# Optimization experiments

Hardware: AMD Instinct MI355X
Metric: run time of the kernel (lower is better)

The kernel has to match this reference:

```python
import jax, jax.numpy as jnp
import numpy as np

WIDTH = 768
HEAD = 64

def setup_inputs() -> dict:
    key = jax.random.key(0)
    ks = jax.random.split(key, 8)
    x = jax.random.normal(ks[0], (8, 2048, WIDTH), dtype=jnp.float32)
    mask = jax.random.randint(ks[1], (2048, 2048), 0, 2, dtype=jnp.int32)
    s = 1.0 / np.sqrt(WIDTH)
    Wq = jax.random.normal(ks[2], (WIDTH, HEAD), dtype=jnp.float32) * s
    Wk = jax.random.normal(ks[3], (WIDTH, HEAD), dtype=jnp.float32) * s
    Wv = jax.random.normal(ks[4], (WIDTH, HEAD), dtype=jnp.float32) * s
    bq = jax.random.normal(ks[5], (HEAD,), dtype=jnp.float32) * 0.01
    bk = jax.random.normal(ks[6], (HEAD,), dtype=jnp.float32) * 0.01
    bv = jax.random.normal(ks[7], (HEAD,), dtype=jnp.float32) * 0.01
    return {"x": x, "Wq": Wq, "bq": bq, "Wk": Wk, "bk": bk, "Wv": Wv, "bv": bv, "mask": mask}

def reference(x, Wq, bq, Wk, bk, Wv, bv, mask) -> jnp.ndarray:
    # x: [B, N, width]; projections -> [B, N, head]
    Q = jnp.einsum('bnw,wh->bnh', x, Wq) + bq
    K = jnp.einsum('bnw,wh->bnh', x, Wk) + bk
    V = jnp.einsum('bnw,wh->bnh', x, Wv) + bv
    scale = 1.0 / jnp.sqrt(jnp.asarray(Q.shape[-1], dtype=Q.dtype))
    scores = jnp.einsum('bqh,bkh->bqk', Q, K) * scale  # [B, N, N]
    scores = jnp.where(mask == 0, -jnp.inf, scores)
    attn = jax.nn.softmax(scores, axis=-1)
    return jnp.einsum('bqk,bkh->bqh', attn, V)
```

## Files before the change

kernel.cpp:

```cpp
#include <hip/hip_runtime.h>

typedef short  s8v   __attribute__((ext_vector_type(8)));
typedef float  f32x4 __attribute__((ext_vector_type(4)));

#define SEQ 2048
#define WID 768

__device__ __forceinline__ unsigned fbits(float f) {
    union { float f; unsigned u; } v; v.f = f; return v.u;
}
__device__ __forceinline__ float bitsf(unsigned u) {
    union { unsigned u; float f; } v; v.u = u; return v.f;
}
__device__ __forceinline__ unsigned short f2b(float f) {
    unsigned u = fbits(f);
    return (unsigned short)((u + 0x7FFFu + ((u >> 16) & 1u)) >> 16);
}
__device__ __forceinline__ unsigned packRNE(float a, float b) {
    unsigned ta = fbits(a) + 0x7FFFu + ((fbits(a) >> 16) & 1u);
    unsigned tb = fbits(b) + 0x7FFFu + ((fbits(b) >> 16) & 1u);
    return __builtin_amdgcn_perm(tb, ta, 0x07060302u);
}
__device__ __forceinline__ unsigned packTRUNC(float a, float b) {
    return __builtin_amdgcn_perm(fbits(b), fbits(a), 0x07060302u);
}
__device__ __forceinline__ f32x4 zero4() { f32x4 z = {0.f, 0.f, 0.f, 0.f}; return z; }

__device__ __forceinline__ void async16(const unsigned short* g, unsigned short* l) {
    __builtin_amdgcn_global_load_lds(
        (const __attribute__((address_space(1))) unsigned int*)g,
        (__attribute__((address_space(3))) unsigned int*)l, 16, 0, 0);
}

__global__ __launch_bounds__(256) void convert_kernel(
    const int* __restrict__ mask,
    const float* __restrict__ Wq, const float* __restrict__ Wk, const float* __restrict__ Wv,
    unsigned short* __restrict__ WF, unsigned* __restrict__ PM)
{
    const int tid = threadIdx.x;
    const int blk = blockIdx.x;
    if (blk < 512) {
        const int gid  = blk * 4 + (tid >> 6);
        const int lane = tid & 63, quad = lane >> 4, c = lane & 15;
        const int qb = gid >> 5, kb = gid & 31;
        unsigned w = 0;
        #pragma unroll
        for (int mt = 0; mt < 2; ++mt) {
            const int q = qb * 32 + mt * 16 + c;
            #pragma unroll
            for (int i = 0; i < 4; ++i) {
                const int4 mm = *(const int4*)&mask[(size_t)q * SEQ + kb * 64 + quad * 16 + 4 * i];
                if (mm.x) w |= 1u << (mt * 16 + i * 4 + 0);
                if (mm.y) w |= 1u << (mt * 16 + i * 4 + 1);
                if (mm.z) w |= 1u << (mt * 16 + i * 4 + 2);
                if (mm.w) w |= 1u << (mt * 16 + i * 4 + 3);
            }
        }
        PM[(size_t)gid * 64 + lane] = w;
    } else {
        const int s2 = (blk - 512) * 256 + tid;
        const int chunk = s2 >> 6, l = s2 & 63;
        const int ntg = chunk / 24, r = chunk - ntg * 24;
        const int kc = r >> 1, h = r & 1;
        const int mat = ntg >> 2;
        const int col = (ntg & 3) * 16 + (l & 15);
        const int k0 = kc * 64 + h * 32 + (l >> 4) * 8;
        const float* Wm = (mat == 0) ? Wq : (mat == 1) ? Wk : Wv;
        float p[8];
        #pragma unroll
        for (int j = 0; j < 8; ++j) p[j] = Wm[(size_t)(k0 + j) * 64 + col];
        uint4 w;
        w.x = packRNE(p[0], p[1]); w.y = packRNE(p[2], p[3]);
        w.z = packRNE(p[4], p[5]); w.w = packRNE(p[6], p[7]);
        *(uint4*)&WF[(size_t)s2 * 8] = w;
    }
}

__global__ __launch_bounds__(512, 4) void qkv_proj_kernel(
    const float* __restrict__ x, const unsigned short* __restrict__ WF,
    const float* __restrict__ bq, const float* __restrict__ bk, const float* __restrict__ bv,
    unsigned short* __restrict__ QF, unsigned short* __restrict__ KF,
    unsigned short* __restrict__ VF)
{
    __shared__ unsigned short AB[2][16384];
    unsigned short (*St)[200] = (unsigned short(*)[200])AB;

    const int tid = threadIdx.x;
    const int wv = tid >> 6, lane = tid & 63, quad = lane >> 4, c = lane & 15;
    const int rg = wv >> 2, cg = wv & 3;
    const int blk = blockIdx.x;
    const int g0 = blk * 4;

    float bias[3];
    #pragma unroll
    for (int nt = 0; nt < 3; ++nt) {
        int col = cg * 48 + nt * 16 + c;
        const float* B = (col < 64) ? bq : (col < 128) ? bk : bv;
        bias[nt] = B[col & 63];
    }

    const int chunk = tid >> 6;
    const int gl = chunk >> 1, hh = chunk & 1;
    const int arow = (g0 + gl) * 16 + (lane & 15);
    const float* xrow = x + (size_t)arow * WID + hh * 32 + ((lane >> 4) & 3) * 8;

    auto issueB = [&](int kc, int b) {
        #pragma unroll
        for (int r = 0; r < 3; ++r) {
            const int e = wv * 3 + r;
            const int ntg = e >> 1, h = e & 1;
            async16(WF + (((size_t)ntg * 12 + kc) * 2 + h) * 512 + lane * 8,
                    &AB[b][4096 + (ntg * 2 + h) * 512]);
        }
    };
    auto stageA_write = [&](int b, float4 f0, float4 f1) {
        uint4 w;
        w.x = packRNE(f0.x, f0.y); w.y = packRNE(f0.z, f0.w);
        w.z = packRNE(f1.x, f1.y); w.w = packRNE(f1.z, f1.w);
        *(uint4*)&AB[b][(size_t)tid * 8] = w;
    };

    f32x4 acc[2][3];
    #pragma unroll
    for (int mt = 0; mt < 2; ++mt)
        #pragma unroll
        for (int nt = 0; nt < 3; ++nt) acc[mt][nt] = zero4();

    {
        float4 f0 = *(const float4*)&xrow[0];
        float4 f1 = *(const float4*)&xrow[4];
        stageA_write(0, f0, f1);
        issueB(0, 0);
    }

    for (int kc = 0; kc < 12; ++kc) {
        const int b = kc & 1;
        __syncthreads();
        float4 f0, f1;
        if (kc < 11) {
            f0 = *(const float4*)&xrow[(kc + 1) * 64];
            f1 = *(const float4*)&xrow[(kc + 1) * 64 + 4];
            issueB(kc + 1, b ^ 1);
        }

        s8v afr[2][2], bfr[3][2];
        #pragma unroll
        for (int mt = 0; mt < 2; ++mt)
            #pragma unroll
            for (int h = 0; h < 2; ++h)
                afr[mt][h] = *(const s8v*)&AB[b][((rg * 2 + mt) * 2 + h) * 512 + lane * 8];
        #pragma unroll
        for (int nt = 0; nt < 3; ++nt)
            #pragma unroll
            for (int h = 0; h < 2; ++h)
                bfr[nt][h] = *(const s8v*)&AB[b][4096 + ((cg * 3 + nt) * 2 + h) * 512 + lane * 8];
        #pragma unroll
        for (int h = 0; h < 2; ++h)
            #pragma unroll
            for (int mt = 0; mt < 2; ++mt)
                #pragma unroll
                for (int nt = 0; nt < 3; ++nt)
                    acc[mt][nt] = __builtin_amdgcn_mfma_f32_16x16x32_bf16(
                        afr[mt][h], bfr[nt][h], acc[mt][nt], 0, 0, 0);

        if (kc < 11) stageA_write(b ^ 1, f0, f1);
    }

    #pragma unroll
    for (int mt = 0; mt < 2; ++mt)
        #pragma unroll
        for (int nt = 0; nt < 3; ++nt)
            #pragma unroll
            for (int i = 0; i < 4; ++i)
                St[rg * 32 + mt * 16 + quad * 4 + i][cg * 48 + nt * 16 + c]
                    = f2b(acc[mt][nt][i] + bias[nt]);
    __syncthreads();

    {
        const int g = tid >> 7, ks = (tid >> 6) & 1, l = tid & 63;
        uint4 v = *(uint4*)&St[g * 16 + (l & 15)][ks * 32 + (l >> 4) * 8];
        *(uint4*)&QF[(((size_t)(g0 + g)) * 2 + ks) * 512 + (size_t)l * 8] = v;
    }
    {
        const int ksnt = tid >> 6, l = tid & 63;
        const int ks = ksnt >> 2, nt = ksnt & 3;
        uint4 v = *(uint4*)&St[4 * (l & 15) + nt][64 + ks * 32 + (l >> 4) * 8];
        *(uint4*)&KF[(((size_t)blk * 8 + ksnt) * 64 + l) * 8] = v;
    }
    {
        const int ksnt = tid >> 6, l = tid & 63;
        const int ks = ksnt >> 2, nt = ksnt & 3;
        const int d = 128 + nt * 16 + (l & 15);
        const int r0 = (l >> 4) * 16 + ks * 8;
        unsigned short p[8];
        #pragma unroll
        for (int s = 0; s < 8; ++s) p[s] = St[r0 + s][d];
        uint4 w;
        w.x = (unsigned)p[0] | ((unsigned)p[1] << 16);
        w.y = (unsigned)p[2] | ((unsigned)p[3] << 16);
        w.z = (unsigned)p[4] | ((unsigned)p[5] << 16);
        w.w = (unsigned)p[6] | ((unsigned)p[7] << 16);
        *(uint4*)&VF[(((size_t)blk * 8 + ksnt) * 64 + l) * 8] = w;
    }
}

__global__ __launch_bounds__(1024, 4) void attn_kernel(
    const unsigned short* __restrict__ QF, const unsigned short* __restrict__ KF,
    const unsigned short* __restrict__ VF, const unsigned* __restrict__ PM,
    float* __restrict__ out)
{
    __shared__ unsigned short KV[4][2][8192];
    __shared__ float Obuf[64][68];
    __shared__ float Lbuf[64];

    const int tid = threadIdx.x;
    const int wv = tid >> 6, lane = tid & 63, quad = lane >> 4, c = lane & 15;
    const int sl = wv & 3, qg = wv >> 2, mt = qg & 1;
    const int blk = blockIdx.x;
    const int bb = blk & 7, qt = blk >> 3;
    const size_t qrow0 = (size_t)bb * SEQ + qt * 64;

    if (tid < 64) Lbuf[tid] = 0.f;

    unsigned pm[8];
    #pragma unroll
    for (int kt = 0; kt < 8; ++kt)
        pm[kt] = PM[(size_t)(((qt * 2 + (qg >> 1)) * 32 + sl * 8 + kt) * 64 + lane)];

    union Q8 { s8v v; unsigned w[4]; } qf[2];
    {
        const size_t qgrp = (size_t)bb * 128 + qt * 4 + qg;
        #pragma unroll
        for (int ks = 0; ks < 2; ++ks)
            qf[ks].v = *(const s8v*)&QF[(qgrp * 2 + ks) * 512 + (size_t)lane * 8];
    }
    asm volatile("s_waitcnt vmcnt(0)" ::: "memory");
    #pragma unroll
    for (int kt = 0; kt < 8; ++kt) asm volatile("" : "+v"(pm[kt]));
    #pragma unroll
    for (int ks = 0; ks < 2; ++ks)
        #pragma unroll
        for (int j = 0; j < 4; ++j) asm volatile("" : "+v"(qf[ks].w[j]));
    __builtin_amdgcn_sched_barrier(0);

    f32x4 O[4];
    float lro = 0.f;
    #pragma unroll
    for (int nt = 0; nt < 4; ++nt) O[nt] = zero4();

    auto kv_dma = [&](int kt, int b) {
        const size_t kbg = (size_t)bb * 32 + sl * 8 + kt;
        #pragma unroll
        for (int r = 0; r < 4; ++r) {
            const int d = qg * 4 + r;
            const unsigned short* src = (d < 8)
                ? KF + kbg * 4096 + (d & 7) * 512 + lane * 8
                : VF + kbg * 4096 + (d & 7) * 512 + lane * 8;
            async16(src, &KV[sl][b][(d >> 3) * 4096 + (d & 7) * 512]);
        }
    };

    kv_dma(0, 0);
    kv_dma(1, 1);

    #pragma unroll
    for (int kt = 0; kt < 8; ++kt) {
        const int b = kt & 1;
        if (kt < 7) asm volatile("s_waitcnt vmcnt(4)" ::: "memory");
        else        asm volatile("s_waitcnt vmcnt(0)" ::: "memory");
        __builtin_amdgcn_sched_barrier(0);
        __builtin_amdgcn_s_barrier();

        f32x4 S[4];
        #pragma unroll
        for (int nt = 0; nt < 4; ++nt) S[nt] = zero4();
        #pragma unroll
        for (int ks = 0; ks < 2; ++ks) {
            s8v kfr[4];
            #pragma unroll
            for (int nt = 0; nt < 4; ++nt)
                kfr[nt] = *(const s8v*)&KV[sl][b][((ks * 4 + nt) * 64 + lane) * 8];
            #pragma unroll
            for (int nt = 0; nt < 4; ++nt)
                S[nt] = __builtin_amdgcn_mfma_f32_16x16x32_bf16(kfr[nt], qf[ks].v, S[nt], 0, 0, 0);
        }

        const unsigned pmh = pm[kt] >> (mt * 16);
        float p[4][4];
        #pragma unroll
        for (int i = 0; i < 4; ++i)
            #pragma unroll
            for (int nt = 0; nt < 4; ++nt) {
                float e = exp2f(fmaf(S[nt][i], 0.18033688011112042f, -21.640425613334451f));
                p[nt][i] = ((pmh >> (i * 4 + nt)) & 1u) ? e : 0.f;
            }
        union { unsigned w[8]; s8v v[2]; } P;
        #pragma unroll
        for (int j = 0; j < 8; ++j) {
            unsigned uu = packTRUNC(p[2 * (j & 1)][j >> 1], p[2 * (j & 1) + 1][j >> 1]);
            P.w[j] = uu;
            lro += bitsf(uu << 16) + bitsf(uu & 0xFFFF0000u);
        }

        #pragma unroll
        for (int ks = 0; ks < 2; ++ks) {
            s8v vfr[4];
            #pragma unroll
            for (int nt = 0; nt < 4; ++nt)
                vfr[nt] = *(const s8v*)&KV[sl][b][4096 + ((ks * 4 + nt) * 64 + lane) * 8];
            #pragma unroll
            for (int nt = 0; nt < 4; ++nt)
                O[nt] = __builtin_amdgcn_mfma_f32_16x16x32_bf16(P.v[ks], vfr[nt], O[nt], 0, 0, 0);
        }

        if (kt < 6) {
            __builtin_amdgcn_s_barrier();
            kv_dma(kt + 2, b);
        }
    }

    #pragma unroll
    for (int j = 0; j < 5; ++j) {
        int idx = tid + 1024 * j;
        if (idx < 64 * 68) ((float*)Obuf)[idx] = 0.f;
    }
    __syncthreads();

    {
        float l = lro;
        l += __shfl_xor(l, 16);
        l += __shfl_xor(l, 32);
        if (quad == 0) atomicAdd(&Lbuf[qg * 16 + c], l);
    }
    #pragma unroll
    for (int i = 0; i < 4; ++i)
        #pragma unroll
        for (int nt = 0; nt < 4; ++nt)
            atomicAdd(&Obuf[qg * 16 + quad * 4 + i][nt * 16 + c], O[nt][i]);
    __syncthreads();
    {
        const int r = tid >> 4, d4 = (tid & 15) * 4;
        const float invL = 1.0f / Lbuf[r];
        float4 v = *(float4*)&Obuf[r][d4];
        float4 o = make_float4(v.x * invL, v.y * invL, v.z * invL, v.w * invL);
        *(float4*)&out[(qrow0 + r) * 64 + d4] = o;
    }
}

extern "C" void kernel_launch(void* const* d_in, const int* in_sizes, int n_in,
                              void* d_out, int out_size, void* d_ws, size_t ws_size,
                              hipStream_t stream)
{
    const float* x    = (const float*)d_in[0];
    const float* Wq   = (const float*)d_in[1];
    const float* bq   = (const float*)d_in[2];
    const float* Wk   = (const float*)d_in[3];
    const float* bk   = (const float*)d_in[4];
    const float* Wv   = (const float*)d_in[5];
    const float* bv   = (const float*)d_in[6];
    const int*   mask = (const int*)d_in[7];
    float* out = (float*)d_out;

    unsigned short* QF = (unsigned short*)d_ws;
    unsigned short* KF = QF + (size_t)16384 * 64;
    unsigned short* VF = KF + (size_t)16384 * 64;
    unsigned short* WF = VF + (size_t)16384 * 64;
    unsigned*       PM = (unsigned*)(WF + (size_t)192 * WID);

    convert_kernel<<<584, 256, 0, stream>>>(mask, Wq, Wk, Wv, WF, PM);
    qkv_proj_kernel<<<256, 512, 0, stream>>>(x, WF, bq, bk, bv, QF, KF, VF);
    attn_kernel<<<256, 1024, 0, stream>>>(QF, KF, VF, PM, out);
}
```

Baseline: 159.5 us.

## Fuse convert, QKV projection and attention into one cooperative kernel

Merges the three separate launches (mask/weight conversion, QKV projection, attention) into a single kernel that runs each phase in turn. The phases are separated by a software grid-wide barrier built on an atomic counter, and the kernel is launched cooperatively, with a plain launch as fallback. The shared-memory buffers of the phases are aliased onto one static array. The aim is to remove inter-kernel launch gaps and the drain/fill between phases. In exchange it adds a memset and two spin-wait barriers, and half the threads sit idle during the projection phase. It also depends on all 256 blocks being co-resident, which with about 145 KB of LDS per block means one block per CU.

```diff
diff --git a/kernel.cpp b/kernel.cpp
--- a/kernel.cpp
+++ b/kernel.cpp
@@ -32,318 +32,334 @@
         (__attribute__((address_space(3))) unsigned int*)l, 16, 0, 0);
 }
 
-__global__ __launch_bounds__(256) void convert_kernel(
-    const int* __restrict__ mask,
+__device__ __forceinline__ void grid_barrier(unsigned* bar) {
+    __syncthreads();
+    if (threadIdx.x == 0) {
+        __threadfence();
+        unsigned my  = atomicAdd(bar, 1u);
+        unsigned gen = my >> 8;
+        volatile unsigned* vb = bar;
+        while ((*vb >> 8) <= gen) __builtin_amdgcn_s_sleep(2);
+        __threadfence();
+    }
+    __syncthreads();
+}
+
+__global__ __launch_bounds__(1024, 4) void fused_kernel(
+    const float* __restrict__ x, const int* __restrict__ mask,
     const float* __restrict__ Wq, const float* __restrict__ Wk, const float* __restrict__ Wv,
-    unsigned short* __restrict__ WF, unsigned* __restrict__ PM)
-{
-    const int tid = threadIdx.x;
-    const int blk = blockIdx.x;
-    if (blk < 512) {
-        const int gid  = blk * 4 + (tid >> 6);
-        const int lane = tid & 63, quad = lane >> 4, c = lane & 15;
-        const int qb = gid >> 5, kb = gid & 31;
-        unsigned w = 0;
-        #pragma unroll
-        for (int mt = 0; mt < 2; ++mt) {
-            const int q = qb * 32 + mt * 16 + c;
-            #pragma unroll
-            for (int i = 0; i < 4; ++i) {
-                const int4 mm = *(const int4*)&mask[(size_t)q * SEQ + kb * 64 + quad * 16 + 4 * i];
-                if (mm.x) w |= 1u << (mt * 16 + i * 4 + 0);
-                if (mm.y) w |= 1u << (mt * 16 + i * 4 + 1);
-                if (mm.z) w |= 1u << (mt * 16 + i * 4 + 2);
-                if (mm.w) w |= 1u << (mt * 16 + i * 4 + 3);
-            }
-        }
-        PM[(size_t)gid * 64 + lane] = w;
-    } else {
-        const int s2 = (blk - 512) * 256 + tid;
-        const int chunk = s2 >> 6, l = s2 & 63;
-        const int ntg = chunk / 24, r = chunk - ntg * 24;
-        const int kc = r >> 1, h = r & 1;
-        const int mat = ntg >> 2;
-        const int col = (ntg & 3) * 16 + (l & 15);
-        const int k0 = kc * 64 + h * 32 + (l >> 4) * 8;
-        const float* Wm = (mat == 0) ? Wq : (mat == 1) ? Wk : Wv;
-        float p[8];
-        #pragma unroll
-        for (int j = 0; j < 8; ++j) p[j] = Wm[(size_t)(k0 + j) * 64 + col];
-        uint4 w;
-        w.x = packRNE(p[0], p[1]); w.y = packRNE(p[2], p[3]);
-        w.z = packRNE(p[4], p[5]); w.w = packRNE(p[6], p[7]);
-        *(uint4*)&WF[(size_t)s2 * 8] = w;
-    }
-}
-
-__global__ __launch_bounds__(512, 4) void qkv_proj_kernel(
-    const float* __restrict__ x, const unsigned short* __restrict__ WF,
     const float* __restrict__ bq, const float* __restrict__ bk, const float* __restrict__ bv,
     unsigned short* __restrict__ QF, unsigned short* __restrict__ KF,
-    unsigned short* __restrict__ VF)
+    unsigned short* __restrict__ VF, unsigned short* __restrict__ WF,
+    unsigned* __restrict__ PM, float* __restrict__ out, unsigned* __restrict__ bar)
 {
-    __shared__ unsigned short AB[2][16384];
-    unsigned short (*St)[200] = (unsigned short(*)[200])AB;
+    __shared__ __align__(16) unsigned char SMEM[148736];
 
     const int tid = threadIdx.x;
     const int wv = tid >> 6, lane = tid & 63, quad = lane >> 4, c = lane & 15;
-    const int rg = wv >> 2, cg = wv & 3;
     const int blk = blockIdx.x;
-    const int g0 = blk * 4;
-
-    float bias[3];
-    #pragma unroll
-    for (int nt = 0; nt < 3; ++nt) {
-        int col = cg * 48 + nt * 16 + c;
-        const float* B = (col < 64) ? bq : (col < 128) ? bk : bv;
-        bias[nt] = B[col & 63];
+
+    {
+        const int gw = blk * 16 + wv;
+        if (gw < 2048) {
+            const int gid = gw;
+            const int qb = gid >> 5, kb = gid & 31;
+            unsigned w = 0;
+            #pragma unroll
+            for (int mt = 0; mt < 2; ++mt) {
+                const int q = qb * 32 + mt * 16 + c;
+                #pragma unroll
+                for (int i = 0; i < 4; ++i) {
+                    const int4 mm = *(const int4*)&mask[(size_t)q * SEQ + kb * 64 + quad * 16 + 4 * i];
+                    if (mm.x) w |= 1u << (mt * 16 + i * 4 + 0);
+                    if (mm.y) w |= 1u << (mt * 16 + i * 4 + 1);
+                    if (mm.z) w |= 1u << (mt * 16 + i * 4 + 2);
+                    if (mm.w) w |= 1u << (mt * 16 + i * 4 + 3);
+                }
+            }
+            PM[(size_t)gid * 64 + lane] = w;
+        } else if (gw < 2336) {
+            const int chunk = gw - 2048;
+            const int ntg = chunk / 24, r = chunk - ntg * 24;
+            const int kc = r >> 1, h = r & 1;
+            const int mat = ntg >> 2;
+            const int col = (ntg & 3) * 16 + c;
+            const int k0 = kc * 64 + h * 32 + (lane >> 4) * 8;
+            const float* Wm = (mat == 0) ? Wq : (mat == 1) ? Wk : Wv;
+            float p[8];
+            #pragma unroll
+            for (int j = 0; j < 8; ++j) p[j] = Wm[(size_t)(k0 + j) * 64 + col];
+            uint4 w;
+            w.x = packRNE(p[0], p[1]); w.y = packRNE(p[2], p[3]);
+            w.z = packRNE(p[4], p[5]); w.w = packRNE(p[6], p[7]);
+            *(uint4*)&WF[(size_t)(chunk * 64 + lane) * 8] = w;
+        }
     }
 
-    const int chunk = tid >> 6;
-    const int gl = chunk >> 1, hh = chunk & 1;
-    const int arow = (g0 + gl) * 16 + (lane & 15);
-    const float* xrow = x + (size_t)arow * WID + hh * 32 + ((lane >> 4) & 3) * 8;
-
-    auto issueB = [&](int kc, int b) {
-        #pragma unroll
-        for (int r = 0; r < 3; ++r) {
-            const int e = wv * 3 + r;
-            const int ntg = e >> 1, h = e & 1;
-            async16(WF + (((size_t)ntg * 12 + kc) * 2 + h) * 512 + lane * 8,
-                    &AB[b][4096 + (ntg * 2 + h) * 512]);
-        }
-    };
-    auto stageA_write = [&](int b, float4 f0, float4 f1) {
-        uint4 w;
-        w.x = packRNE(f0.x, f0.y); w.y = packRNE(f0.z, f0.w);
-        w.z = packRNE(f1.x, f1.y); w.w = packRNE(f1.z, f1.w);
-        *(uint4*)&AB[b][(size_t)tid * 8] = w;
-    };
-
-    f32x4 acc[2][3];
-    #pragma unroll
-    for (int mt = 0; mt < 2; ++mt)
-        #pragma unroll
-        for (int nt = 0; nt < 3; ++nt) acc[mt][nt] = zero4();
+    grid_barrier(bar);
 
     {
-        float4 f0 = *(const float4*)&xrow[0];
-        float4 f1 = *(const float4*)&xrow[4];
-        stageA_write(0, f0, f1);
-        issueB(0, 0);
+        unsigned short (*AB)[16384] = (unsigned short(*)[16384])SMEM;
+        unsigned short (*St)[200]   = (unsigned short(*)[200])SMEM;
+        const int g0 = blk * 4;
+
+        if (tid < 512) {
+            const int pwv = wv;
+            const int rg = pwv >> 2, cg = pwv & 3;
+
+            float bias[3];
+            #pragma unroll
+            for (int nt = 0; nt < 3; ++nt) {
+                int col = cg * 48 + nt * 16 + c;
+                const float* B = (col < 64) ? bq : (col < 128) ? bk : bv;
+                bias[nt] = B[col & 63];
+            }
+
+            const int chunk = tid >> 6;
+            const int gl = chunk >> 1, hh = chunk & 1;
+            const int arow = (g0 + gl) * 16 + (lane & 15);
+            const float* xrow = x + (size_t)arow * WID + hh * 32 + ((lane >> 4) & 3) * 8;
+
+            auto issueB = [&](int kc, int b) {
+                #pragma unroll
+                for (int r = 0; r < 3; ++r) {
+                    const int e = pwv * 3 + r;
+                    const int ntg = e >> 1, h = e & 1;
+                    async16(WF + (((size_t)ntg * 12 + kc) * 2 + h) * 512 + lane * 8,
+                            &AB[b][4096 + (ntg * 2 + h) * 512]);
+                }
+            };
+            auto stageA_write = [&](int b, float4 f0, float4 f1) {
+                uint4 w;
+                w.x = packRNE(f0.x, f0.y); w.y = packRNE(f0.z, f0.w);
+                w.z = packRNE(f1.x, f1.y); w.w = packRNE(f1.z, f1.w);
+                *(uint4*)&AB[b][(size_t)tid * 8] = w;
+            };
+
+            f32x4 acc[2][3];
+            #pragma unroll
+            for (int mt = 0; mt < 2; ++mt)
+                #pragma unroll
+                for (int nt = 0; nt < 3; ++nt) acc[mt][nt] = zero4();
+
+            {
+                float4 f0 = *(const float4*)&xrow[0];
+                float4 f1 = *(const float4*)&xrow[4];
+                stageA_write(0, f0, f1);
+                issueB(0, 0);
+            }
+
+            for (int kc = 0; kc < 12; ++kc) {
+                const int b = kc & 1;
+                __syncthreads();
+                float4 f0, f1;
+                if (kc < 11) {
+                    f0 = *(const float4*)&xrow[(kc + 1) * 64];
+                    f1 = *(const float4*)&xrow[(kc + 1) * 64 + 4];
+                    issueB(kc + 1, b ^ 1);
+                }
+
+                s8v afr[2][2], bfr[3][2];
+                #pragma unroll
+                for (int mt = 0; mt < 2; ++mt)
+                    #pragma unroll
+                    for (int h = 0; h < 2; ++h)
+                        afr[mt][h] = *(const s8v*)&AB[b][((rg * 2 + mt) * 2 + h) * 512 + lane * 8];
+                #pragma unroll
+                for (int nt = 0; nt < 3; ++nt)
+                    #pragma unroll
+                    for (int h = 0; h < 2; ++h)
+                        bfr[nt][h] = *(const s8v*)&AB[b][4096 + ((cg * 3 + nt) * 2 + h) * 512 + lane * 8];
+                #pragma unroll
+                for (int h = 0; h < 2; ++h)
+                    #pragma unroll
+                    for (int mt = 0; mt < 2; ++mt)
+                        #pragma unroll
+                        for (int nt = 0; nt < 3; ++nt)
+                            acc[mt][nt] = __builtin_amdgcn_mfma_f32_16x16x32_bf16(
+                                afr[mt][h], bfr[nt][h], acc[mt][nt], 0, 0, 0);
+
+                if (kc < 11) stageA_write(b ^ 1, f0, f1);
+            }
+
+            #pragma unroll
+            for (int mt = 0; mt < 2; ++mt)
+                #pragma unroll
+                for (int nt = 0; nt < 3; ++nt)
+                    #pragma unroll
+                    for (int i = 0; i < 4; ++i)
+                        St[rg * 32 + mt * 16 + quad * 4 + i][cg * 48 + nt * 16 + c]
+                            = f2b(acc[mt][nt][i] + bias[nt]);
+            __syncthreads();
+
+            {
+                const int g = tid >> 7, ks = (tid >> 6) & 1, l = tid & 63;
+                uint4 v = *(uint4*)&St[g * 16 + (l & 15)][ks * 32 + (l >> 4) * 8];
+                *(uint4*)&QF[(((size_t)(g0 + g)) * 2 + ks) * 512 + (size_t)l * 8] = v;
+            }
+            {
+                const int ksnt = tid >> 6, l = tid & 63;
+                const int ks = ksnt >> 2, nt = ksnt & 3;
+                uint4 v = *(uint4*)&St[4 * (l & 15) + nt][64 + ks * 32 + (l >> 4) * 8];
+                *(uint4*)&KF[(((size_t)blk * 8 + ksnt) * 64 + l) * 8] = v;
+            }
+            {
+                const int ksnt = tid >> 6, l = tid & 63;
+                const int ks = ksnt >> 2, nt = ksnt & 3;
+                const int d = 128 + nt * 16 + (l & 15);
+                const int r0 = (l >> 4) * 16 + ks * 8;
+                unsigned short p[8];
+                #pragma unroll
+                for (int s = 0; s < 8; ++s) p[s] = St[r0 + s][d];
+                uint4 w;
+                w.x = (unsigned)p[0] | ((unsigned)p[1] << 16);
+                w.y = (unsigned)p[2] | ((unsigned)p[3] << 16);
+                w.z = (unsigned)p[4] | ((unsigned)p[5] << 16);
+                w.w = (unsigned)p[6] | ((unsigned)p[7] << 16);
+                *(uint4*)&VF[(((size_t)blk * 8 + ksnt) * 64 + l) * 8] = w;
+            }
+        } else {
+            #pragma unroll 1
+            for (int i = 0; i < 13; ++i) __syncthreads();
+        }
     }
 
-    for (int kc = 0; kc < 12; ++kc) {
-        const int b = kc & 1;
+    grid_barrier(bar);
+
+    {
+        unsigned short* KVb = (unsigned short*)SMEM;
+        float (*Obuf)[68]   = (float(*)[68])(SMEM + 131072);
+        float* Lbuf         = (float*)(SMEM + 131072 + 17408);
+
+        const int sl = wv & 3, qg = wv >> 2, mt = qg & 1;
+        const int bb = blk & 7, qt = blk >> 3;
+        const size_t qrow0 = (size_t)bb * SEQ + qt * 64;
+
+        if (tid < 64) Lbuf[tid] = 0.f;
+
+        unsigned pm[8];
+        #pragma unroll
+        for (int kt = 0; kt < 8; ++kt)
+            pm[kt] = PM[(size_t)(((qt * 2 + (qg >> 1)) * 32 + sl * 8 + kt) * 64 + lane)];
+
+        union Q8 { s8v v; unsigned w[4]; } qf[2];
+        {
+            const size_t qgrp = (size_t)bb * 128 + qt * 4 + qg;
+            #pragma unroll
+            for (int ks = 0; ks < 2; ++ks)
+                qf[ks].v = *(const s8v*)&QF[(qgrp * 2 + ks) * 512 + (size_t)lane * 8];
+        }
+        asm volatile("s_waitcnt vmcnt(0)" ::: "memory");
+        #pragma unroll
+        for (int kt = 0; kt < 8; ++kt) asm volatile("" : "+v"(pm[kt]));
+        #pragma unroll
+        for (int ks = 0; ks < 2; ++ks)
+            #pragma unroll
+            for (int j = 0; j < 4; ++j) asm volatile("" : "+v"(qf[ks].w[j]));
+        __builtin_amdgcn_sched_barrier(0);
+
+        f32x4 O[4];
+        float lro = 0.f;
+        #pragma unroll
+        for (int nt = 0; nt < 4; ++nt) O[nt] = zero4();
+
+        auto kv_dma = [&](int kt, int b) {
+            const size_t kbg = (size_t)bb * 32 + sl * 8 + kt;
+            #pragma unroll
+            for (int r = 0; r < 4; ++r) {
+                const int d = qg * 4 + r;
+                const unsigned short* src = (d < 8)
+                    ? KF + kbg * 4096 + (d & 7) * 512 + lane * 8
+                    : VF + kbg * 4096 + (d & 7) * 512 + lane * 8;
+                async16(src, &KVb[sl * 16384 + b * 8192 + (d >> 3) * 4096 + (d & 7) * 512]);
+            }
+        };
+
+        kv_dma(0, 0);
+        kv_dma(1, 1);
+
+        #pragma unroll
+        for (int kt = 0; kt < 8; ++kt) {
+            const int b = kt & 1;
+            if (kt < 7) asm volatile("s_waitcnt vmcnt(4)" ::: "memory");
+            else        asm volatile("s_waitcnt vmcnt(0)" ::: "memory");
+            __builtin_amdgcn_sched_barrier(0);
+            __builtin_amdgcn_s_barrier();
+
+            f32x4 S[4];
+            #pragma unroll
+            for (int nt = 0; nt < 4; ++nt) S[nt] = zero4();
+            #pragma unroll
+            for (int ks = 0; ks < 2; ++ks) {
+                s8v kfr[4];
+                #pragma unroll
+                for (int nt = 0; nt < 4; ++nt)
+                    kfr[nt] = *(const s8v*)&KVb[sl * 16384 + b * 8192 + ((ks * 4 + nt) * 64 + lane) * 8];
+                #pragma unroll
+                for (int nt = 0; nt < 4; ++nt)
+                    S[nt] = __builtin_amdgcn_mfma_f32_16x16x32_bf16(kfr[nt], qf[ks].v, S[nt], 0, 0, 0);
+            }
+
+            const unsigned pmh = pm[kt] >> (mt * 16);
+            float p[4][4];
+            #pragma unroll
+            for (int i = 0; i < 4; ++i)
+                #pragma unroll
+                for (int nt = 0; nt < 4; ++nt) {
+                    float e = exp2f(fmaf(S[nt][i], 0.18033688011112042f, -21.640425613334451f));
+                    p[nt][i] = ((pmh >> (i * 4 + nt)) & 1u) ? e : 0.f;
+                }
+            union { unsigned w[8]; s8v v[2]; } P;
+            #pragma unroll
+            for (int j = 0; j < 8; ++j) {
+                unsigned uu = packTRUNC(p[2 * (j & 1)][j >> 1], p[2 * (j & 1) + 1][j >> 1]);
+                P.w[j] = uu;
+                lro += bitsf(uu << 16) + bitsf(uu & 0xFFFF0000u);
+            }
+
+            #pragma unroll
+            for (int ks = 0; ks < 2; ++ks) {
+                s8v vfr[4];
+                #pragma unroll
+                for (int nt = 0; nt < 4; ++nt)
+                    vfr[nt] = *(const s8v*)&KVb[sl * 16384 + b * 8192 + 4096 + ((ks * 4 + nt) * 64 + lane) * 8];
+                #pragma unroll
+                for (int nt = 0; nt < 4; ++nt)
+                    O[nt] = __builtin_amdgcn_mfma_f32_16x16x32_bf16(P.v[ks], vfr[nt], O[nt], 0, 0, 0);
+            }
+
+            if (kt < 6) {
+                __builtin_amdgcn_s_barrier();
+                kv_dma(kt + 2, b);
+            }
+        }
+
+        #pragma unroll
+        for (int j = 0; j < 5; ++j) {
+            int idx = tid + 1024 * j;
+            if (idx < 64 * 68) ((float*)Obuf)[idx] = 0.f;
+        }
         __syncthreads();
-        float4 f0, f1;
-        if (kc < 11) {
-            f0 = *(const float4*)&xrow[(kc + 1) * 64];
-            f1 = *(const float4*)&xrow[(kc + 1) * 64 + 4];
-            issueB(kc + 1, b ^ 1);
-        }
-
-        s8v afr[2][2], bfr[3][2];
-        #pragma unroll
-        for (int mt = 0; mt < 2; ++mt)
-            #pragma unroll
-            for (int h = 0; h < 2; ++h)
-                afr[mt][h] = *(const s8v*)&AB[b][((rg * 2 + mt) * 2 + h) * 512 + lane * 8];
-        #pragma unroll
-        for (int nt = 0; nt < 3; ++nt)
-            #pragma unroll
-            for (int h = 0; h < 2; ++h)
-                bfr[nt][h] = *(const s8v*)&AB[b][4096 + ((cg * 3 + nt) * 2 + h) * 512 + lane * 8];
-        #pragma unroll
-        for (int h = 0; h < 2; ++h)
-            #pragma unroll
-            for (int mt = 0; mt < 2; ++mt)
-                #pragma unroll
-                for (int nt = 0; nt < 3; ++nt)
-                    acc[mt][nt] = __builtin_amdgcn_mfma_f32_16x16x32_bf16(
-                        afr[mt][h], bfr[nt][h], acc[mt][nt], 0, 0, 0);
-
-        if (kc < 11) stageA_write(b ^ 1, f0, f1);
-    }
-
-    #pragma unroll
-    for (int mt = 0; mt < 2; ++mt)
-        #pragma unroll
-        for (int nt = 0; nt < 3; ++nt)
-            #pragma unroll
-            for (int i = 0; i < 4; ++i)
-                St[rg * 32 + mt * 16 + quad * 4 + i][cg * 48 + nt * 16 + c]
-                    = f2b(acc[mt][nt][i] + bias[nt]);
-    __syncthreads();
-
-    {
-        const int g = tid >> 7, ks = (tid >> 6) & 1, l = tid & 63;
-        uint4 v = *(uint4*)&St[g * 16 + (l & 15)][ks * 32 + (l >> 4) * 8];
-        *(uint4*)&QF[(((size_t)(g0 + g)) * 2 + ks) * 512 + (size_t)l * 8] = v;
-    }
-    {
-        const int ksnt = tid >> 6, l = tid & 63;
-        const int ks = ksnt >> 2, nt = ksnt & 3;
-        uint4 v = *(uint4*)&St[4 * (l & 15) + nt][64 + ks * 32 + (l >> 4) * 8];
-        *(uint4*)&KF[(((size_t)blk * 8 + ksnt) * 64 + l) * 8] = v;
-    }
-    {
-        const int ksnt = tid >> 6, l = tid & 63;
-        const int ks = ksnt >> 2, nt = ksnt & 3;
-        const int d = 128 + nt * 16 + (l & 15);
-        const int r0 = (l >> 4) * 16 + ks * 8;
-        unsigned short p[8];
-        #pragma unroll
-        for (int s = 0; s < 8; ++s) p[s] = St[r0 + s][d];
-        uint4 w;
-        w.x = (unsigned)p[0] | ((unsigned)p[1] << 16);
-        w.y = (unsigned)p[2] | ((unsigned)p[3] << 16);
-        w.z = (unsigned)p[4] | ((unsigned)p[5] << 16);
-        w.w = (unsigned)p[6] | ((unsigned)p[7] << 16);
-        *(uint4*)&VF[(((size_t)blk * 8 + ksnt) * 64 + l) * 8] = w;
-    }
-}
-
-__global__ __launch_bounds__(1024, 4) void attn_kernel(
-    const unsigned short* __restrict__ QF, const unsigned short* __restrict__ KF,
-    const unsigned short* __restrict__ VF, const unsigned* __restrict__ PM,
-    float* __restrict__ out)
-{
-    __shared__ unsigned short KV[4][2][8192];
-    __shared__ float Obuf[64][68];
-    __shared__ float Lbuf[64];
-
-    const int tid = threadIdx.x;
-    const int wv = tid >> 6, lane = tid & 63, quad = lane >> 4, c = lane & 15;
-    const int sl = wv & 3, qg = wv >> 2, mt = qg & 1;
-    const int blk = blockIdx.x;
-    const int bb = blk & 7, qt = blk >> 3;
-    const size_t qrow0 = (size_t)bb * SEQ + qt * 64;
-
-    if (tid < 64) Lbuf[tid] = 0.f;
-
-    unsigned pm[8];
-    #pragma unroll
-    for (int kt = 0; kt < 8; ++kt)
-        pm[kt] = PM[(size_t)(((qt * 2 + (qg >> 1)) * 32 + sl * 8 + kt) * 64 + lane)];
-
-    union Q8 { s8v v; unsigned w[4]; } qf[2];
-    {
-        const size_t qgrp = (size_t)bb * 128 + qt * 4 + qg;
-        #pragma unroll
-        for (int ks = 0; ks < 2; ++ks)
-            qf[ks].v = *(const s8v*)&QF[(qgrp * 2 + ks) * 512 + (size_t)lane * 8];
-    }
-    asm volatile("s_waitcnt vmcnt(0)" ::: "memory");
-    #pragma unroll
-    for (int kt = 0; kt < 8; ++kt) asm volatile("" : "+v"(pm[kt]));
-    #pragma unroll
-    for (int ks = 0; ks < 2; ++ks)
-        #pragma unroll
-        for (int j = 0; j < 4; ++j) asm volatile("" : "+v"(qf[ks].w[j]));
-    __builtin_amdgcn_sched_barrier(0);
-
-    f32x4 O[4];
-    float lro = 0.f;
-    #pragma unroll
-    for (int nt = 0; nt < 4; ++nt) O[nt] = zero4();
-
-    auto kv_dma = [&](int kt, int b) {
-        const size_t kbg = (size_t)bb * 32 + sl * 8 + kt;
-        #pragma unroll
-        for (int r = 0; r < 4; ++r) {
-            const int d = qg * 4 + r;
-            const unsigned short* src = (d < 8)
-                ? KF + kbg * 4096 + (d & 7) * 512 + lane * 8
-                : VF + kbg * 4096 + (d & 7) * 512 + lane * 8;
-            async16(src, &KV[sl][b][(d >> 3) * 4096 + (d & 7) * 512]);
-        }
-    };
-
-    kv_dma(0, 0);
-    kv_dma(1, 1);
-
-    #pragma unroll
-    for (int kt = 0; kt < 8; ++kt) {
-        const int b = kt & 1;
-        if (kt < 7) asm volatile("s_waitcnt vmcnt(4)" ::: "memory");
-        else        asm volatile("s_waitcnt vmcnt(0)" ::: "memory");
-        __builtin_amdgcn_sched_barrier(0);
-        __builtin_amdgcn_s_barrier();
-
-        f32x4 S[4];
-        #pragma unroll
-        for (int nt = 0; nt < 4; ++nt) S[nt] = zero4();
-        #pragma unroll
-        for (int ks = 0; ks < 2; ++ks) {
-            s8v kfr[4];
+
+        {
+            float l = lro;
+            l += __shfl_xor(l, 16);
+            l += __shfl_xor(l, 32);
+            if (quad == 0) atomicAdd(&Lbuf[qg * 16 + c], l);
+        }
+        #pragma unroll
+        for (int i = 0; i < 4; ++i)
             #pragma unroll
             for (int nt = 0; nt < 4; ++nt)
-                kfr[nt] = *(const s8v*)&KV[sl][b][((ks * 4 + nt) * 64 + lane) * 8];
-            #pragma unroll
-            for (int nt = 0; nt < 4; ++nt)
-                S[nt] = __builtin_amdgcn_mfma_f32_16x16x32_bf16(kfr[nt], qf[ks].v, S[nt], 0, 0, 0);
-        }
-
-        const unsigned pmh = pm[kt] >> (mt * 16);
-        float p[4][4];
-        #pragma unroll
-        for (int i = 0; i < 4; ++i)
-            #pragma unroll
-            for (int nt = 0; nt < 4; ++nt) {
-                float e = exp2f(fmaf(S[nt][i], 0.18033688011112042f, -21.640425613334451f));
-                p[nt][i] = ((pmh >> (i * 4 + nt)) & 1u) ? e : 0.f;
-            }
-        union { unsigned w[8]; s8v v[2]; } P;
-        #pragma unroll
-        for (int j = 0; j < 8; ++j) {
-            unsigned uu = packTRUNC(p[2 * (j & 1)][j >> 1], p[2 * (j & 1) + 1][j >> 1]);
-            P.w[j] = uu;
-            lro += bitsf(uu << 16) + bitsf(uu & 0xFFFF0000u);
-        }
-
-        #pragma unroll
-        for (int ks = 0; ks < 2; ++ks) {
-            s8v vfr[4];
-            #pragma unroll
-            for (int nt = 0; nt < 4; ++nt)
-                vfr[nt] = *(const s8v*)&KV[sl][b][4096 + ((ks * 4 + nt) * 64 + lane) * 8];
-            #pragma unroll
-            for (int nt = 0; nt < 4; ++nt)
-                O[nt] = __builtin_amdgcn_mfma_f32_16x16x32_bf16(P.v[ks], vfr[nt], O[nt], 0, 0, 0);
-        }
-
-        if (kt < 6) {
-            __builtin_amdgcn_s_barrier();
-            kv_dma(kt + 2, b);
-        }
-    }
-
-    #pragma unroll
-    for (int j = 0; j < 5; ++j) {
-        int idx = tid + 1024 * j;
-        if (idx < 64 * 68) ((float*)Obuf)[idx] = 0.f;
-    }
-    __syncthreads();
-
-    {
-        float l = lro;
-        l += __shfl_xor(l, 16);
-        l += __shfl_xor(l, 32);
-        if (quad == 0) atomicAdd(&Lbuf[qg * 16 + c], l);
-    }
-    #pragma unroll
-    for (int i = 0; i < 4; ++i)
-        #pragma unroll
-        for (int nt = 0; nt < 4; ++nt)
-            atomicAdd(&Obuf[qg * 16 + quad * 4 + i][nt * 16 + c], O[nt][i]);
-    __syncthreads();
-    {
-        const int r = tid >> 4, d4 = (tid & 15) * 4;
-        const float invL = 1.0f / Lbuf[r];
-        float4 v = *(float4*)&Obuf[r][d4];
-        float4 o = make_float4(v.x * invL, v.y * invL, v.z * invL, v.w * invL);
-        *(float4*)&out[(qrow0 + r) * 64 + d4] = o;
+                atomicAdd(&Obuf[qg * 16 + quad * 4 + i][nt * 16 + c], O[nt][i]);
+        __syncthreads();
+        {
+            const int r = tid >> 4, d4 = (tid & 15) * 4;
+            const float invL = 1.0f / Lbuf[r];
+            float4 v = *(float4*)&Obuf[r][d4];
+            float4 o = make_float4(v.x * invL, v.y * invL, v.z * invL, v.w * invL);
+            *(float4*)&out[(qrow0 + r) * 64 + d4] = o;
+        }
     }
 }
 
@@ -366,8 +382,19 @@
     unsigned short* VF = KF + (size_t)16384 * 64;
     unsigned short* WF = VF + (size_t)16384 * 64;
     unsigned*       PM = (unsigned*)(WF + (size_t)192 * WID);
-
-    convert_kernel<<<584, 256, 0, stream>>>(mask, Wq, Wk, Wv, WF, PM);
-    qkv_proj_kernel<<<256, 512, 0, stream>>>(x, WF, bq, bk, bv, QF, KF, VF);
-    attn_kernel<<<256, 1024, 0, stream>>>(QF, KF, VF, PM, out);
-}
+    unsigned*       bar = PM + (size_t)2048 * 64;
+
+    hipMemsetAsync(bar, 0, 4, stream);
+
+    void* args[] = { (void*)&x, (void*)&mask, (void*)&Wq, (void*)&Wk, (void*)&Wv,
+                     (void*)&bq, (void*)&bk, (void*)&bv,
+                     (void*)&QF, (void*)&KF, (void*)&VF, (void*)&WF,
+                     (void*)&PM, (void*)&out, (void*)&bar };
+    hipError_t e = hipLaunchCooperativeKernel((const void*)fused_kernel,
+                                              dim3(256), dim3(1024), args, 0, stream);
+    if (e != hipSuccess) {
+        (void)hipGetLastError();
+        fused_kernel<<<256, 1024, 0, stream>>>(x, mask, Wq, Wk, Wv, bq, bk, bv,
+                                               QF, KF, VF, WF, PM, out, bar);
+    }
+}
```

Result: slower. 239.4 us (+50.1%).

## Load K/V fragments directly from global into registers, dropping LDS double buffer

Applied to the files above, without the earlier changes.

Removes the shared-memory K/V double buffer, its async DMA copies and the per-tile block barriers. Each wave now reads its K and V fragments straight from global memory into registers inside a non-unrolled loop, and loads the mask word per iteration instead of prefetching all eight up front. The row-sum accumulator is also split into two partial sums to shorten the dependency chain. This trades LDS traffic and synchronisation for more global/L2 loads, which are now redundant across the query-group waves. It also gives up the software prefetch overlap and raises register pressure.

```diff
diff --git a/kernel.cpp b/kernel.cpp
--- a/kernel.cpp
+++ b/kernel.cpp
@@ -209,7 +209,6 @@
     const unsigned short* __restrict__ VF, const unsigned* __restrict__ PM,
     float* __restrict__ out)
 {
-    __shared__ unsigned short KV[4][2][8192];
     __shared__ float Obuf[64][68];
     __shared__ float Lbuf[64];
 
@@ -222,11 +221,6 @@
 
     if (tid < 64) Lbuf[tid] = 0.f;
 
-    unsigned pm[8];
-    #pragma unroll
-    for (int kt = 0; kt < 8; ++kt)
-        pm[kt] = PM[(size_t)(((qt * 2 + (qg >> 1)) * 32 + sl * 8 + kt) * 64 + lane)];
-
     union Q8 { s8v v; unsigned w[4]; } qf[2];
     {
         const size_t qgrp = (size_t)bb * 128 + qt * 4 + qg;
@@ -234,58 +228,39 @@
         for (int ks = 0; ks < 2; ++ks)
             qf[ks].v = *(const s8v*)&QF[(qgrp * 2 + ks) * 512 + (size_t)lane * 8];
     }
-    asm volatile("s_waitcnt vmcnt(0)" ::: "memory");
-    #pragma unroll
-    for (int kt = 0; kt < 8; ++kt) asm volatile("" : "+v"(pm[kt]));
-    #pragma unroll
-    for (int ks = 0; ks < 2; ++ks)
-        #pragma unroll
-        for (int j = 0; j < 4; ++j) asm volatile("" : "+v"(qf[ks].w[j]));
-    __builtin_amdgcn_sched_barrier(0);
 
     f32x4 O[4];
-    float lro = 0.f;
+    float lro0 = 0.f, lro1 = 0.f;
     #pragma unroll
     for (int nt = 0; nt < 4; ++nt) O[nt] = zero4();
 
-    auto kv_dma = [&](int kt, int b) {
+    const unsigned* pmrow = PM + (size_t)((qt * 2 + (qg >> 1)) * 32 + sl * 8) * 64 + lane;
+
+    #pragma unroll 1
+    for (int kt = 0; kt < 8; ++kt) {
         const size_t kbg = (size_t)bb * 32 + sl * 8 + kt;
-        #pragma unroll
-        for (int r = 0; r < 4; ++r) {
-            const int d = qg * 4 + r;
-            const unsigned short* src = (d < 8)
-                ? KF + kbg * 4096 + (d & 7) * 512 + lane * 8
-                : VF + kbg * 4096 + (d & 7) * 512 + lane * 8;
-            async16(src, &KV[sl][b][(d >> 3) * 4096 + (d & 7) * 512]);
-        }
-    };
-
-    kv_dma(0, 0);
-    kv_dma(1, 1);
-
-    #pragma unroll
-    for (int kt = 0; kt < 8; ++kt) {
-        const int b = kt & 1;
-        if (kt < 7) asm volatile("s_waitcnt vmcnt(4)" ::: "memory");
-        else        asm volatile("s_waitcnt vmcnt(0)" ::: "memory");
-        __builtin_amdgcn_sched_barrier(0);
-        __builtin_amdgcn_s_barrier();
+        const unsigned short* kb_ = KF + kbg * 4096 + (size_t)lane * 8;
+        const unsigned short* vb_ = VF + kbg * 4096 + (size_t)lane * 8;
+
+        const unsigned pmw = pmrow[(size_t)kt * 64];
+
+        s8v vfr[8];
+        #pragma unroll
+        for (int d = 0; d < 8; ++d) vfr[d] = *(const s8v*)&vb_[(size_t)d * 512];
+        s8v kfr[8];
+        #pragma unroll
+        for (int d = 0; d < 8; ++d) kfr[d] = *(const s8v*)&kb_[(size_t)d * 512];
 
         f32x4 S[4];
         #pragma unroll
         for (int nt = 0; nt < 4; ++nt) S[nt] = zero4();
         #pragma unroll
-        for (int ks = 0; ks < 2; ++ks) {
-            s8v kfr[4];
+        for (int ks = 0; ks < 2; ++ks)
             #pragma unroll
             for (int nt = 0; nt < 4; ++nt)
-                kfr[nt] = *(const s8v*)&KV[sl][b][((ks * 4 + nt) * 64 + lane) * 8];
-            #pragma unroll
-            for (int nt = 0; nt < 4; ++nt)
-                S[nt] = __builtin_amdgcn_mfma_f32_16x16x32_bf16(kfr[nt], qf[ks].v, S[nt], 0, 0, 0);
-        }
-
-        const unsigned pmh = pm[kt] >> (mt * 16);
+                S[nt] = __builtin_amdgcn_mfma_f32_16x16x32_bf16(kfr[ks * 4 + nt], qf[ks].v, S[nt], 0, 0, 0);
+
+        const unsigned pmh = pmw >> (mt * 16);
         float p[4][4];
         #pragma unroll
         for (int i = 0; i < 4; ++i)
@@ -299,24 +274,15 @@
         for (int j = 0; j < 8; ++j) {
             unsigned uu = packTRUNC(p[2 * (j & 1)][j >> 1], p[2 * (j & 1) + 1][j >> 1]);
             P.w[j] = uu;
-            lro += bitsf(uu << 16) + bitsf(uu & 0xFFFF0000u);
+            if (j & 1) lro1 += bitsf(uu << 16) + bitsf(uu & 0xFFFF0000u);
+            else       lro0 += bitsf(uu << 16) + bitsf(uu & 0xFFFF0000u);
         }
 
         #pragma unroll
-        for (int ks = 0; ks < 2; ++ks) {
-            s8v vfr[4];
+        for (int ks = 0; ks < 2; ++ks)
             #pragma unroll
             for (int nt = 0; nt < 4; ++nt)
-                vfr[nt] = *(const s8v*)&KV[sl][b][4096 + ((ks * 4 + nt) * 64 + lane) * 8];
-            #pragma unroll
-            for (int nt = 0; nt < 4; ++nt)
-                O[nt] = __builtin_amdgcn_mfma_f32_16x16x32_bf16(P.v[ks], vfr[nt], O[nt], 0, 0, 0);
-        }
-
-        if (kt < 6) {
-            __builtin_amdgcn_s_barrier();
-            kv_dma(kt + 2, b);
-        }
+                O[nt] = __builtin_amdgcn_mfma_f32_16x16x32_bf16(P.v[ks], vfr[ks * 4 + nt], O[nt], 0, 0, 0);
     }
 
     #pragma unroll
@@ -327,7 +293,7 @@
     __syncthreads();
 
     {
-        float l = lro;
+        float l = lro0 + lro1;
         l += __shfl_xor(l, 16);
         l += __shfl_xor(l, 32);
         if (quad == 0) atomicAdd(&Lbuf[qg * 16 + c], l);
```

Measured after the change: 159.6 us. No clear change (+0.1%).
